# Performance work log

Hardware: AMD Instinct MI355X
Metric: run time of the kernel (lower is better)

The kernel has to match this reference:

```python
import jax, jax.numpy as jnp
import numpy as np

T, N, F_IN = 5, 10000, 16
E = 160000
C = 32          # gat_hidden_dim (per head)
H0 = 2          # heads in layer 0 (concat) -> out 64
GRU = 64
OUT_H = 32


def setup_inputs() -> dict:
    key = jax.random.key(0)
    ks = jax.random.split(key, 24)
    s = 0.1
    inp = {
        "x_seq": jax.random.normal(ks[0], (T, N, F_IN), jnp.float32),
        "edge_index": jax.random.randint(ks[1], (2, E), 0, N, jnp.int32),
        # GAT layer 0: in 16 -> 2 heads x 32, concat -> 64
        "gat0_W": s * jax.random.normal(ks[2], (F_IN, H0 * C), jnp.float32),
        "gat0_asrc": s * jax.random.normal(ks[3], (H0, C), jnp.float32),
        "gat0_adst": s * jax.random.normal(ks[4], (H0, C), jnp.float32),
        "gat0_b": s * jax.random.normal(ks[5], (H0 * C,), jnp.float32),
        "res0_W": s * jax.random.normal(ks[6], (F_IN, H0 * C), jnp.float32),   # [in,out]
        # GAT layer 1: in 64 -> 1 head x 32, no concat -> 32
        "gat1_W": s * jax.random.normal(ks[7], (H0 * C, C), jnp.float32),
        "gat1_asrc": s * jax.random.normal(ks[8], (1, C), jnp.float32),
        "gat1_adst": s * jax.random.normal(ks[9], (1, C), jnp.float32),
        "gat1_b": s * jax.random.normal(ks[10], (C,), jnp.float32),
        "res1_W": s * jax.random.normal(ks[11], (H0 * C, C), jnp.float32),
        # GRU cells (torch GRUCell layout: W_i [3H,in], W_h [3H,H])
        "gru0_Wi": s * jax.random.normal(ks[12], (3 * GRU, C), jnp.float32),
        "gru0_Wh": s * jax.random.normal(ks[13], (3 * GRU, GRU), jnp.float32),
        "gru0_bi": s * jax.random.normal(ks[14], (3 * GRU,), jnp.float32),
        "gru0_bh": s * jax.random.normal(ks[15], (3 * GRU,), jnp.float32),
        "gru1_Wi": s * jax.random.normal(ks[16], (3 * GRU, GRU), jnp.float32),
        "gru1_Wh": s * jax.random.normal(ks[17], (3 * GRU, GRU), jnp.float32),
        "gru1_bi": s * jax.random.normal(ks[18], (3 * GRU,), jnp.float32),
        "gru1_bh": s * jax.random.normal(ks[19], (3 * GRU,), jnp.float32),
        # MLP head
        "fc1_W": s * jax.random.normal(ks[20], (GRU, OUT_H), jnp.float32),
        "fc1_b": s * jax.random.normal(ks[21], (OUT_H,), jnp.float32),
        "fc2_W": s * jax.random.normal(ks[22], (OUT_H, 1), jnp.float32),
        "fc2_b": s * jax.random.normal(ks[23], (1,), jnp.float32),
    }
    return inp


def _gat(x, src, dst, n, W, a_src, a_dst, b, heads, concat):
    ch = W.shape[1] // heads
    xw = (x @ W).reshape(n, heads, ch)                      # [N,H,C]
    al_s = (xw * a_src).sum(-1)                             # [N,H]
    al_d = (xw * a_dst).sum(-1)
    e = jax.nn.leaky_relu(al_s[src] + al_d[dst], 0.2)       # [Etot,H]
    m = jax.ops.segment_max(e, dst, num_segments=n)
    ex = jnp.exp(e - m[dst])
    den = jax.ops.segment_sum(ex, dst, num_segments=n)
    alpha = ex / (den[dst] + 1e-16)                         # scatter-softmax
    out = jax.ops.segment_sum(alpha[:, :, None] * xw[src], dst, num_segments=n)
    out = out.reshape(n, heads * ch) if concat else out.mean(axis=1)
    return out + b


def _gru(x, h, Wi, Wh, bi, bh):
    gi = x @ Wi.T + bi
    gh = h @ Wh.T + bh
    i_r, i_z, i_n = jnp.split(gi, 3, axis=-1)
    h_r, h_z, h_n = jnp.split(gh, 3, axis=-1)
    r = jax.nn.sigmoid(i_r + h_r)
    z = jax.nn.sigmoid(i_z + h_z)
    nn_ = jnp.tanh(i_n + r * h_n)
    return (1.0 - z) * nn_ + z * h


def reference(x_seq, edge_index,
              gat0_W, gat0_asrc, gat0_adst, gat0_b, res0_W,
              gat1_W, gat1_asrc, gat1_adst, gat1_b, res1_W,
              gru0_Wi, gru0_Wh, gru0_bi, gru0_bh,
              gru1_Wi, gru1_Wh, gru1_bi, gru1_bh,
              fc1_W, fc1_b, fc2_W, fc2_b):
    n = x_seq.shape[1]
    loops = jnp.arange(n, dtype=edge_index.dtype)
    src = jnp.concatenate([edge_index[0], loops])           # PyG adds self-loops
    dst = jnp.concatenate([edge_index[1], loops])

    def step(carry, x_t):
        h0, h1 = carry
        x1 = jax.nn.elu(_gat(x_t, src, dst, n, gat0_W, gat0_asrc, gat0_adst, gat0_b, 2, True)) + x_t @ res0_W
        x2 = jax.nn.elu(_gat(x1, src, dst, n, gat1_W, gat1_asrc, gat1_adst, gat1_b, 1, False)) + x1 @ res1_W
        h0 = _gru(x2, h0, gru0_Wi, gru0_Wh, gru0_bi, gru0_bh)
        h1 = _gru(h0, h1, gru1_Wi, gru1_Wh, gru1_bi, gru1_bh)
        return (h0, h1), None

    h0 = jnp.zeros((n, gru0_Wh.shape[1]), x_seq.dtype)
    h1 = jnp.zeros((n, gru1_Wh.shape[1]), x_seq.dtype)
    (h0, h1), _ = jax.lax.scan(step, (h0, h1), x_seq)
    h = jax.nn.relu(h1 @ fc1_W + fc1_b)
    return h @ fc2_W + fc2_b                                # [N,1]
```

## Files before the change

### kernel.cpp

```cpp
#include <hip/hip_runtime.h>
#include <hip/hip_bf16.h>
#include <math.h>

#define T_STEPS 5
#define NNODES  10000
#define NM      (T_STEPS * NNODES)
#define F_IN    16
#define NEDGES  160000
#define ETOT    (NEDGES + NNODES)
#define GW      8
#define GNPW    5

#define RL(v, k) __int_as_float(__builtin_amdgcn_readlane(__float_as_int(v), (k)))

__global__ __launch_bounds__(256) void k_count(const int* __restrict__ ei, int* __restrict__ counts) {
    int idx = blockIdx.x * 256 + threadIdx.x;
    if (idx >= ETOT) return;
    int dst = (idx < NEDGES) ? ei[NEDGES + idx] : (idx - NEDGES);
    atomicAdd(&counts[dst], 1);
}

__global__ __launch_bounds__(1024) void k_scan(const int* __restrict__ counts, int* __restrict__ offs) {
    __shared__ int ssum[1024];
    int t = threadIdx.x;
    const int chunk = (NNODES + 1023) / 1024;
    int start = t * chunk, end = min(start + chunk, NNODES);
    int s = 0;
    for (int i = start; i < end; i++) s += counts[i];
    ssum[t] = s;
    __syncthreads();
    for (int off = 1; off < 1024; off <<= 1) {
        int v = (t >= off) ? ssum[t - off] : 0;
        __syncthreads();
        ssum[t] += v;
        __syncthreads();
    }
    int excl = (t == 0) ? 0 : ssum[t - 1];
    for (int i = start; i < end; i++) { offs[i] = excl; excl += counts[i]; }
    if (t == 1023) offs[NNODES] = ssum[1023];
}

__global__ __launch_bounds__(256) void k_fill(const int* __restrict__ ei, const int* __restrict__ offs,
                                              int* __restrict__ cursor, int* __restrict__ csr) {
    int idx = blockIdx.x * 256 + threadIdx.x;
    if (idx >= ETOT) return;
    int src, dst;
    if (idx < NEDGES) { src = ei[idx]; dst = ei[NEDGES + idx]; }
    else              { src = dst = idx - NEDGES; }
    int p = atomicAdd(&cursor[dst], 1);
    csr[offs[dst] + p] = src;
}

__global__ __launch_bounds__(256) void k_transpose(const float* __restrict__ Wi0, const float* __restrict__ Wh0,
                                                   const float* __restrict__ Wi1, const float* __restrict__ Wh1,
                                                   float* __restrict__ WiT0, float* __restrict__ WhT0,
                                                   float* __restrict__ WiT1, float* __restrict__ WhT1,
                                                   float4* __restrict__ wp0, float4* __restrict__ hp0,
                                                   float4* __restrict__ ip1, float4* __restrict__ hp1) {
    int idx = blockIdx.x * 256 + threadIdx.x;
    if (idx < 6144)  { int k = idx / 192, r = idx % 192; WiT0[idx] = Wi0[r * 32 + k]; return; }
    idx -= 6144;
    if (idx < 12288) { int k = idx / 192, r = idx % 192; WhT0[idx] = Wh0[r * 64 + k]; return; }
    idx -= 12288;
    if (idx < 12288) { int k = idx / 192, r = idx % 192; WiT1[idx] = Wi1[r * 64 + k]; return; }
    idx -= 12288;
    if (idx < 12288) { int k = idx / 192, r = idx % 192; WhT1[idx] = Wh1[r * 64 + k]; return; }
    idx -= 12288;
    if (idx < 1536) { int k4 = idx / 192, c = idx % 192; const float* s = Wi0 + c * 32 + 4 * k4;
                      wp0[idx] = make_float4(s[0], s[1], s[2], s[3]); return; }
    idx -= 1536;
    if (idx < 3072) { int k4 = idx / 192, c = idx % 192; const float* s = Wh0 + c * 64 + 4 * k4;
                      hp0[idx] = make_float4(s[0], s[1], s[2], s[3]); return; }
    idx -= 3072;
    if (idx < 3072) { int k4 = idx / 192, c = idx % 192; const float* s = Wi1 + c * 64 + 4 * k4;
                      ip1[idx] = make_float4(s[0], s[1], s[2], s[3]); return; }
    idx -= 3072;
    if (idx < 3072) { int k4 = idx / 192, c = idx % 192; const float* s = Wh1 + c * 64 + 4 * k4;
                      hp1[idx] = make_float4(s[0], s[1], s[2], s[3]); }
}

__global__ __launch_bounds__(256) void k_mm0_all(const float* __restrict__ x,
                                                 const float* __restrict__ W,
                                                 const float* __restrict__ Wres,
                                                 const float* __restrict__ asrc,
                                                 const float* __restrict__ adst,
                                                 float* __restrict__ xw, float* __restrict__ xres,
                                                 float* __restrict__ als, float* __restrict__ ald) {
    int wave = threadIdx.x >> 6, lane = threadIdx.x & 63;
    int m = blockIdx.x * 4 + wave;
    if (m >= NM) return;
    const float* xr = x + (size_t)m * F_IN;
    float xreg[F_IN];
#pragma unroll
    for (int k = 0; k < F_IN; k++) xreg[k] = xr[k];
    float acc = 0.f, accr = 0.f;
#pragma unroll
    for (int k = 0; k < F_IN; k++) {
        acc  += xreg[k] * W[k * 64 + lane];
        accr += xreg[k] * Wres[k * 64 + lane];
    }
    xw[(size_t)m * 64 + lane]   = acc;
    xres[(size_t)m * 64 + lane] = accr;
    float ps = acc * asrc[lane], pd = acc * adst[lane];
    for (int off = 16; off; off >>= 1) {
        ps += __shfl_down(ps, off, 32);
        pd += __shfl_down(pd, off, 32);
    }
    if ((lane & 31) == 0) {
        int h = lane >> 5;
        als[m * 2 + h] = ps;
        ald[m * 2 + h] = pd;
    }
}

__global__ __launch_bounds__(256) void k_gat0_all(const float* __restrict__ xw,
                                                  const float* __restrict__ xres,
                                                  const float* __restrict__ als,
                                                  const float* __restrict__ ald,
                                                  const int* __restrict__ offs, const int* __restrict__ csr,
                                                  const float* __restrict__ b,
                                                  const float* __restrict__ W1,
                                                  const float* __restrict__ Wres1,
                                                  const float* __restrict__ as1,
                                                  const float* __restrict__ ad1v,
                                                  float* __restrict__ xw1, float* __restrict__ xres1,
                                                  float* __restrict__ als1, float* __restrict__ ald1) {
    int wave = threadIdx.x >> 6, lane = threadIdx.x & 63;
    int m = blockIdx.x * 4 + wave;
    if (m >= NM) return;
    int t = m / NNODES;
    int node = m - t * NNODES;
    int base = t * NNODES;
    int beg = offs[node], end = offs[node + 1];
    int deg = end - beg;
    float ad0 = ald[m * 2 + 0], ad1 = ald[m * 2 + 1];
    float acc;
    if (deg <= 64) {
        int s = 0; float e0 = -INFINITY, e1 = -INFINITY;
        if (lane < deg) {
            s = base + csr[beg + lane];
            e0 = als[s * 2 + 0] + ad0; e0 = e0 > 0.f ? e0 : 0.2f * e0;
            e1 = als[s * 2 + 1] + ad1; e1 = e1 > 0.f ? e1 : 0.2f * e1;
        }
        float m0 = e0, m1 = e1;
        for (int o = 32; o; o >>= 1) {
            m0 = fmaxf(m0, __shfl_xor(m0, o));
            m1 = fmaxf(m1, __shfl_xor(m1, o));
        }
        float ex0 = (lane < deg) ? __expf(e0 - m0) : 0.f;
        float ex1 = (lane < deg) ? __expf(e1 - m1) : 0.f;
        float d0 = ex0, d1 = ex1;
        for (int o = 32; o; o >>= 1) {
            d0 += __shfl_xor(d0, o);
            d1 += __shfl_xor(d1, o);
        }
        ex0 *= 1.f / (d0 + 1e-16f);
        ex1 *= 1.f / (d1 + 1e-16f);
        float a0 = 0.f, a1 = 0.f, a2 = 0.f, a3 = 0.f;
        int i = 0;
        for (; i + 4 <= deg; i += 4) {
            int   s0 = __shfl(s, i),     s1 = __shfl(s, i + 1), s2 = __shfl(s, i + 2), s3 = __shfl(s, i + 3);
            float u0 = __shfl(ex0, i),   v0 = __shfl(ex1, i);
            float u1 = __shfl(ex0, i+1), v1 = __shfl(ex1, i+1);
            float u2 = __shfl(ex0, i+2), v2 = __shfl(ex1, i+2);
            float u3 = __shfl(ex0, i+3), v3 = __shfl(ex1, i+3);
            a0 += (lane < 32 ? u0 : v0) * xw[(size_t)s0 * 64 + lane];
            a1 += (lane < 32 ? u1 : v1) * xw[(size_t)s1 * 64 + lane];
            a2 += (lane < 32 ? u2 : v2) * xw[(size_t)s2 * 64 + lane];
            a3 += (lane < 32 ? u3 : v3) * xw[(size_t)s3 * 64 + lane];
        }
        for (; i < deg; i++) {
            int s0 = __shfl(s, i);
            float u = __shfl(ex0, i), v = __shfl(ex1, i);
            a0 += (lane < 32 ? u : v) * xw[(size_t)s0 * 64 + lane];
        }
        acc = (a0 + a1) + (a2 + a3);
    } else {
        float m0 = -INFINITY, m1 = -INFINITY;
        for (int i = beg + lane; i < end; i += 64) {
            int s = base + csr[i];
            float e0 = als[s * 2 + 0] + ad0; e0 = e0 > 0.f ? e0 : 0.2f * e0;
            float e1 = als[s * 2 + 1] + ad1; e1 = e1 > 0.f ? e1 : 0.2f * e1;
            m0 = fmaxf(m0, e0); m1 = fmaxf(m1, e1);
        }
        for (int o = 32; o; o >>= 1) {
            m0 = fmaxf(m0, __shfl_xor(m0, o));
            m1 = fmaxf(m1, __shfl_xor(m1, o));
        }
        float d0 = 0.f, d1 = 0.f;
        for (int i = beg + lane; i < end; i += 64) {
            int s = base + csr[i];
            float e0 = als[s * 2 + 0] + ad0; e0 = e0 > 0.f ? e0 : 0.2f * e0;
            float e1 = als[s * 2 + 1] + ad1; e1 = e1 > 0.f ? e1 : 0.2f * e1;
            d0 += __expf(e0 - m0); d1 += __expf(e1 - m1);
        }
        for (int o = 32; o; o >>= 1) { d0 += __shfl_xor(d0, o); d1 += __shfl_xor(d1, o); }
        float inv0 = 1.f / (d0 + 1e-16f), inv1 = 1.f / (d1 + 1e-16f);
        acc = 0.f;
        for (int i = beg; i < end; i++) {
            int s = base + csr[i];
            float e, wgt;
            if (lane < 32) { e = als[s * 2 + 0] + ad0; e = e > 0.f ? e : 0.2f * e; wgt = __expf(e - m0) * inv0; }
            else           { e = als[s * 2 + 1] + ad1; e = e > 0.f ? e : 0.2f * e; wgt = __expf(e - m1) * inv1; }
            acc += wgt * xw[(size_t)s * 64 + lane];
        }
    }
    float x1v = acc + b[lane];
    x1v = x1v > 0.f ? x1v : expm1f(x1v);
    x1v += xres[(size_t)m * 64 + lane];
    int j = lane & 31;
    const float* Wp = (lane < 32) ? W1 : Wres1;
    float pacc = 0.f;
#pragma unroll
    for (int k = 0; k < 64; k++) {
        float xv = RL(x1v, k);
        pacc += xv * Wp[k * 32 + j];
    }
    if (lane < 32) xw1[(size_t)m * 32 + j]   = pacc;
    else           xres1[(size_t)m * 32 + j] = pacc;
    float ps = (lane < 32) ? pacc * as1[j]  : 0.f;
    float pd = (lane < 32) ? pacc * ad1v[j] : 0.f;
    for (int o = 16; o; o >>= 1) {
        ps += __shfl_down(ps, o, 32);
        pd += __shfl_down(pd, o, 32);
    }
    if (lane == 0) { als1[m] = ps; ald1[m] = pd; }
}

__global__ __launch_bounds__(256) void k_gat1_all(const float* __restrict__ xw1,
                                                  const float* __restrict__ xres1,
                                                  const float* __restrict__ als1,
                                                  const float* __restrict__ ald1,
                                                  const int* __restrict__ offs, const int* __restrict__ csr,
                                                  const float* __restrict__ b,
                                                  float* __restrict__ x2) {
    int wave = threadIdx.x >> 6, lane = threadIdx.x & 63;
    int m = blockIdx.x * 4 + wave;
    if (m >= NM) return;
    int t = m / NNODES;
    int node = m - t * NNODES;
    int base = t * NNODES;
    int beg = offs[node], end = offs[node + 1];
    int deg = end - beg;
    float adv = ald1[m];
    int ch = lane & 31, half = lane >> 5;
    float aggr;
    if (deg <= 64) {
        int s = 0; float e = -INFINITY;
        if (lane < deg) {
            s = base + csr[beg + lane];
            e = als1[s] + adv; e = e > 0.f ? e : 0.2f * e;
        }
        float mx = e;
        for (int o = 32; o; o >>= 1) mx = fmaxf(mx, __shfl_xor(mx, o));
        float ex = (lane < deg) ? __expf(e - mx) : 0.f;
        float d = ex;
        for (int o = 32; o; o >>= 1) d += __shfl_xor(d, o);
        ex *= 1.f / (d + 1e-16f);
        float acc = 0.f;
        for (int i = 0; i < deg; i += 2) {
            int i2 = (i + 1 < deg) ? i + 1 : i;
            int   sa = __shfl(s, i),  sb = __shfl(s, i2);
            float wa = __shfl(ex, i), wb = __shfl(ex, i2);
            if (i + 1 >= deg) wb = 0.f;
            int   sm = half ? sb : sa;
            float wm = half ? wb : wa;
            acc += wm * xw1[(size_t)sm * 32 + ch];
        }
        acc += __shfl_xor(acc, 32);
        aggr = acc;
    } else {
        float mx = -INFINITY;
        for (int i = beg + lane; i < end; i += 64) {
            float e = als1[base + csr[i]] + adv; e = e > 0.f ? e : 0.2f * e;
            mx = fmaxf(mx, e);
        }
        for (int o = 32; o; o >>= 1) mx = fmaxf(mx, __shfl_xor(mx, o));
        float d = 0.f;
        for (int i = beg + lane; i < end; i += 64) {
            float e = als1[base + csr[i]] + adv; e = e > 0.f ? e : 0.2f * e;
            d += __expf(e - mx);
        }
        for (int o = 32; o; o >>= 1) d += __shfl_xor(d, o);
        float inv = 1.f / (d + 1e-16f);
        float acc = 0.f;
        for (int i = beg; i < end; i++) {
            int s = base + csr[i];
            float e = als1[s] + adv; e = e > 0.f ? e : 0.2f * e;
            float wgt = __expf(e - mx) * inv;
            acc += wgt * xw1[(size_t)s * 32 + ch];
        }
        aggr = acc;
    }
    if (lane < 32) {
        float v = aggr + b[ch];
        v = v > 0.f ? v : expm1f(v);
        x2[(size_t)m * 32 + ch] = v + xres1[(size_t)m * 32 + ch];
    }
}

__global__ __launch_bounds__(512) void k_gruhead_p(const float* __restrict__ x2,
                                                   const float4* __restrict__ wp0,
                                                   const float4* __restrict__ hp0,
                                                   const float4* __restrict__ ip1,
                                                   const float4* __restrict__ hp1,
                                                   const float* __restrict__ bi0, const float* __restrict__ bh0,
                                                   const float* __restrict__ bi1, const float* __restrict__ bh1,
                                                   const float* __restrict__ fc1W, const float* __restrict__ fc1b,
                                                   const float* __restrict__ fc2W, const float* __restrict__ fc2b,
                                                   float* __restrict__ out) {
    extern __shared__ float4 lds4[];
    float4* Lh0 = lds4;
    float4* Li1 = lds4 + 3072;
    float4* Lh1 = lds4 + 6144;
    int tid = threadIdx.x, wave = tid >> 6, lane = tid & 63;
    int node0 = (blockIdx.x * GW + wave) * GNPW;

    for (int i = tid; i < 3072; i += 512) { Lh0[i] = hp0[i]; Li1[i] = ip1[i]; Lh1[i] = hp1[i]; }
    __syncthreads();

    float bir0 = bi0[lane] + bh0[lane];
    float biz0 = bi0[64 + lane] + bh0[64 + lane];
    float bin0 = bi0[128 + lane], bhn0 = bh0[128 + lane];
    float bir1 = bi1[lane] + bh1[lane];
    float biz1 = bi1[64 + lane] + bh1[64 + lane];
    float bin1 = bi1[128 + lane], bhn1 = bh1[128 + lane];

    float h0[GNPW] = {0.f, 0.f, 0.f, 0.f, 0.f};
    float h1[GNPW] = {0.f, 0.f, 0.f, 0.f, 0.f};

    for (int t = 0; t < T_STEPS; t++) {
        size_t rb = ((size_t)t * NNODES + node0) * 32;
        float xa = x2[rb + lane];
        float xb = x2[rb + 64 + lane];
        float xc = x2[rb + 128 + (lane & 31)];

        float gr[GNPW], gz[GNPW], gin[GNPW], ghn[GNPW];
#pragma unroll
        for (int n = 0; n < GNPW; n++) { gr[n] = bir0; gz[n] = biz0; gin[n] = bin0; ghn[n] = bhn0; }
#pragma unroll
        for (int k4 = 0; k4 < 8; k4++) {
            float4 wr = wp0[(k4 * 3 + 0) * 64 + lane];
            float4 wz = wp0[(k4 * 3 + 1) * 64 + lane];
            float4 wn = wp0[(k4 * 3 + 2) * 64 + lane];
            int kb = 4 * k4;
#pragma unroll
            for (int n = 0; n < GNPW; n++) {
                float x0, x1, x2v, x3;
                if      (n == 0) { x0 = RL(xa, kb); x1 = RL(xa, kb+1); x2v = RL(xa, kb+2); x3 = RL(xa, kb+3); }
                else if (n == 1) { x0 = RL(xa, 32+kb); x1 = RL(xa, 33+kb); x2v = RL(xa, 34+kb); x3 = RL(xa, 35+kb); }
                else if (n == 2) { x0 = RL(xb, kb); x1 = RL(xb, kb+1); x2v = RL(xb, kb+2); x3 = RL(xb, kb+3); }
                else if (n == 3) { x0 = RL(xb, 32+kb); x1 = RL(xb, 33+kb); x2v = RL(xb, 34+kb); x3 = RL(xb, 35+kb); }
                else             { x0 = RL(xc, kb); x1 = RL(xc, kb+1); x2v = RL(xc, kb+2); x3 = RL(xc, kb+3); }
                gr[n]  += x0 * wr.x + x1 * wr.y + x2v * wr.z + x3 * wr.w;
                gz[n]  += x0 * wz.x + x1 * wz.y + x2v * wz.z + x3 * wz.w;
                gin[n] += x0 * wn.x + x1 * wn.y + x2v * wn.z + x3 * wn.w;
            }
        }
#pragma unroll 4
        for (int k4 = 0; k4 < 16; k4++) {
            float4 wr = Lh0[(k4 * 3 + 0) * 64 + lane];
            float4 wz = Lh0[(k4 * 3 + 1) * 64 + lane];
            float4 wn = Lh0[(k4 * 3 + 2) * 64 + lane];
            int kb = 4 * k4;
#pragma unroll
            for (int n = 0; n < GNPW; n++) {
                float x0 = RL(h0[n], kb), x1 = RL(h0[n], kb+1), x2v = RL(h0[n], kb+2), x3 = RL(h0[n], kb+3);
                gr[n]  += x0 * wr.x + x1 * wr.y + x2v * wr.z + x3 * wr.w;
                gz[n]  += x0 * wz.x + x1 * wz.y + x2v * wz.z + x3 * wz.w;
                ghn[n] += x0 * wn.x + x1 * wn.y + x2v * wn.z + x3 * wn.w;
            }
        }
#pragma unroll
        for (int n = 0; n < GNPW; n++) {
            float r = 1.f / (1.f + __expf(-gr[n]));
            float z = 1.f / (1.f + __expf(-gz[n]));
            float nn = tanhf(gin[n] + r * ghn[n]);
            h0[n] = (1.f - z) * nn + z * h0[n];
        }

#pragma unroll
        for (int n = 0; n < GNPW; n++) { gr[n] = bir1; gz[n] = biz1; gin[n] = bin1; }
#pragma unroll 4
        for (int k4 = 0; k4 < 16; k4++) {
            float4 wr = Li1[(k4 * 3 + 0) * 64 + lane];
            float4 wz = Li1[(k4 * 3 + 1) * 64 + lane];
            float4 wn = Li1[(k4 * 3 + 2) * 64 + lane];
            int kb = 4 * k4;
#pragma unroll
            for (int n = 0; n < GNPW; n++) {
                float x0 = RL(h0[n], kb), x1 = RL(h0[n], kb+1), x2v = RL(h0[n], kb+2), x3 = RL(h0[n], kb+3);
                gr[n]  += x0 * wr.x + x1 * wr.y + x2v * wr.z + x3 * wr.w;
                gz[n]  += x0 * wz.x + x1 * wz.y + x2v * wz.z + x3 * wz.w;
                gin[n] += x0 * wn.x + x1 * wn.y + x2v * wn.z + x3 * wn.w;
            }
        }
#pragma unroll
        for (int n = 0; n < GNPW; n++) ghn[n] = bhn1;
#pragma unroll 4
        for (int k4 = 0; k4 < 16; k4++) {
            float4 wr = Lh1[(k4 * 3 + 0) * 64 + lane];
            float4 wz = Lh1[(k4 * 3 + 1) * 64 + lane];
            float4 wn = Lh1[(k4 * 3 + 2) * 64 + lane];
            int kb = 4 * k4;
#pragma unroll
            for (int n = 0; n < GNPW; n++) {
                float x0 = RL(h1[n], kb), x1 = RL(h1[n], kb+1), x2v = RL(h1[n], kb+2), x3 = RL(h1[n], kb+3);
                gr[n]  += x0 * wr.x + x1 * wr.y + x2v * wr.z + x3 * wr.w;
                gz[n]  += x0 * wz.x + x1 * wz.y + x2v * wz.z + x3 * wz.w;
                ghn[n] += x0 * wn.x + x1 * wn.y + x2v * wn.z + x3 * wn.w;
            }
        }
#pragma unroll
        for (int n = 0; n < GNPW; n++) {
            float r = 1.f / (1.f + __expf(-gr[n]));
            float z = 1.f / (1.f + __expf(-gz[n]));
            float nn = tanhf(gin[n] + r * ghn[n]);
            h1[n] = (1.f - z) * nn + z * h1[n];
        }
    }

    int j = lane & 31, half = lane >> 5;
#pragma unroll
    for (int p = 0; p < 3; p++) {
        int ne = 2 * p;
        int no = (2 * p + 1 < GNPW) ? 2 * p + 1 : 2 * p;
        float a = fc1b[j];
#pragma unroll
        for (int k = 0; k < 64; k++) {
            float he = RL(h1[ne], k);
            float ho = RL(h1[no], k);
            a += (half ? ho : he) * fc1W[k * 32 + j];
        }
        a = fmaxf(a, 0.f);
        float v = a * fc2W[j];
        for (int o = 16; o; o >>= 1) v += __shfl_down(v, o, 32);
        if ((lane & 31) == 0 && 2 * p + half < GNPW) out[node0 + 2 * p + half] = v + fc2b[0];
    }
}

__global__ __launch_bounds__(512) void k_gruhead(const float* __restrict__ x2,
                                                 const float* __restrict__ WiT0,
                                                 const float* __restrict__ WhT0,
                                                 const float* __restrict__ WiT1,
                                                 const float* __restrict__ WhT1,
                                                 const float* __restrict__ bi0, const float* __restrict__ bh0,
                                                 const float* __restrict__ bi1, const float* __restrict__ bh1,
                                                 const float* __restrict__ fc1W, const float* __restrict__ fc1b,
                                                 const float* __restrict__ fc2W, const float* __restrict__ fc2b,
                                                 float* __restrict__ out) {
    __shared__ float lw[64 * 192];
    int tid = threadIdx.x;
    int wave = tid >> 6, lane = tid & 63;
    int node0 = (blockIdx.x * GW + wave) * GNPW;

    float bir0 = bi0[lane] + bh0[lane];
    float biz0 = bi0[64 + lane] + bh0[64 + lane];
    float bin0 = bi0[128 + lane], bhn0 = bh0[128 + lane];
    float bir1 = bi1[lane] + bh1[lane];
    float biz1 = bi1[64 + lane] + bh1[64 + lane];
    float bin1 = bi1[128 + lane], bhn1 = bh1[128 + lane];

    float h0[GNPW] = {0.f, 0.f, 0.f, 0.f, 0.f};
    float h1[GNPW] = {0.f, 0.f, 0.f, 0.f, 0.f};

    auto stage = [&](const float* __restrict__ src) {
        __syncthreads();
        const float4* s4 = (const float4*)src;
        float4* d4 = (float4*)lw;
#pragma unroll
        for (int i = 0; i < 6; i++) d4[tid + i * 512] = s4[tid + i * 512];
        __syncthreads();
    };

    for (int t = 0; t < T_STEPS; t++) {
        size_t rb = ((size_t)t * NNODES + node0) * 32;
        float xa = x2[rb + lane];
        float xb = x2[rb + 64 + lane];
        float xc = x2[rb + 128 + (lane & 31)];

        float gr[GNPW], gz[GNPW], gin[GNPW], ghn[GNPW];
#pragma unroll
        for (int n = 0; n < GNPW; n++) { gr[n] = bir0; gz[n] = biz0; gin[n] = bin0; ghn[n] = bhn0; }
#pragma unroll 4
        for (int k = 0; k < 32; k++) {
            float wr = WiT0[k * 192 + lane];
            float wz = WiT0[k * 192 + 64 + lane];
            float wn = WiT0[k * 192 + 128 + lane];
            float xv[GNPW];
            xv[0] = RL(xa, k); xv[1] = RL(xa, 32 + k);
            xv[2] = RL(xb, k); xv[3] = RL(xb, 32 + k);
            xv[4] = RL(xc, k);
#pragma unroll
            for (int n = 0; n < GNPW; n++) {
                gr[n] += xv[n] * wr; gz[n] += xv[n] * wz; gin[n] += xv[n] * wn;
            }
        }
        stage(WhT0);
#pragma unroll 4
        for (int k = 0; k < 64; k++) {
            float wr = lw[k * 192 + lane];
            float wz = lw[k * 192 + 64 + lane];
            float wn = lw[k * 192 + 128 + lane];
#pragma unroll
            for (int n = 0; n < GNPW; n++) {
                float hv = RL(h0[n], k);
                gr[n] += hv * wr; gz[n] += hv * wz; ghn[n] += hv * wn;
            }
        }
#pragma unroll
        for (int n = 0; n < GNPW; n++) {
            float r = 1.f / (1.f + __expf(-gr[n]));
            float z = 1.f / (1.f + __expf(-gz[n]));
            float nn = tanhf(gin[n] + r * ghn[n]);
            h0[n] = (1.f - z) * nn + z * h0[n];
        }
#pragma unroll
        for (int n = 0; n < GNPW; n++) { gr[n] = bir1; gz[n] = biz1; gin[n] = bin1; }
        stage(WiT1);
#pragma unroll 4
        for (int k = 0; k < 64; k++) {
            float wir = lw[k * 192 + lane];
            float wiz = lw[k * 192 + 64 + lane];
            float win = lw[k * 192 + 128 + lane];
#pragma unroll
            for (int n = 0; n < GNPW; n++) {
                float xv = RL(h0[n], k);
                gr[n] += xv * wir; gz[n] += xv * wiz; gin[n] += xv * win;
            }
        }
#pragma unroll
        for (int n = 0; n < GNPW; n++) ghn[n] = bhn1;
        stage(WhT1);
#pragma unroll 4
        for (int k = 0; k < 64; k++) {
            float whr = lw[k * 192 + lane];
            float whz = lw[k * 192 + 64 + lane];
            float whn = lw[k * 192 + 128 + lane];
#pragma unroll
            for (int n = 0; n < GNPW; n++) {
                float hv = RL(h1[n], k);
                gr[n] += hv * whr; gz[n] += hv * whz; ghn[n] += hv * whn;
            }
        }
#pragma unroll
        for (int n = 0; n < GNPW; n++) {
            float r = 1.f / (1.f + __expf(-gr[n]));
            float z = 1.f / (1.f + __expf(-gz[n]));
            float nn = tanhf(gin[n] + r * ghn[n]);
            h1[n] = (1.f - z) * nn + z * h1[n];
        }
    }

    int j = lane & 31, half = lane >> 5;
#pragma unroll
    for (int p = 0; p < 3; p++) {
        int ne = 2 * p;
        int no = (2 * p + 1 < GNPW) ? 2 * p + 1 : 2 * p;
        float a = fc1b[j];
#pragma unroll
        for (int k = 0; k < 64; k++) {
            float he = RL(h1[ne], k);
            float ho = RL(h1[no], k);
            a += (half ? ho : he) * fc1W[k * 32 + j];
        }
        a = fmaxf(a, 0.f);
        float v = a * fc2W[j];
        for (int o = 16; o; o >>= 1) v += __shfl_down(v, o, 32);
        if ((lane & 31) == 0 && 2 * p + half < GNPW) out[node0 + 2 * p + half] = v + fc2b[0];
    }
}

extern "C" void kernel_launch(void* const* d_in, const int* in_sizes, int n_in,
                              void* d_out, int out_size, void* d_ws, size_t ws_size,
                              hipStream_t stream) {
    const float* x_seq   = (const float*)d_in[0];
    const int*   ei      = (const int*)d_in[1];
    const float* gat0_W  = (const float*)d_in[2];
    const float* gat0_as = (const float*)d_in[3];
    const float* gat0_ad = (const float*)d_in[4];
    const float* gat0_b  = (const float*)d_in[5];
    const float* res0_W  = (const float*)d_in[6];
    const float* gat1_W  = (const float*)d_in[7];
    const float* gat1_as = (const float*)d_in[8];
    const float* gat1_ad = (const float*)d_in[9];
    const float* gat1_b  = (const float*)d_in[10];
    const float* res1_W  = (const float*)d_in[11];
    const float* gru0_Wi = (const float*)d_in[12];
    const float* gru0_Wh = (const float*)d_in[13];
    const float* gru0_bi = (const float*)d_in[14];
    const float* gru0_bh = (const float*)d_in[15];
    const float* gru1_Wi = (const float*)d_in[16];
    const float* gru1_Wh = (const float*)d_in[17];
    const float* gru1_bi = (const float*)d_in[18];
    const float* gru1_bh = (const float*)d_in[19];
    const float* fc1_W   = (const float*)d_in[20];
    const float* fc1_b   = (const float*)d_in[21];
    const float* fc2_W   = (const float*)d_in[22];
    const float* fc2_b   = (const float*)d_in[23];
    float* out = (float*)d_out;

    char* w = (char*)d_ws;
    size_t off = 0;
    auto take = [&](size_t bytes) { size_t r = off; off += (bytes + 255) & ~(size_t)255; return r; };
    const size_t N = NNODES, M = NM;
    int*    counts = (int*)(w + take(N * 4));
    int*    cursor = (int*)(w + take(N * 4));
    int*    offs   = (int*)(w + take((N + 1) * 4));
    int*    csr    = (int*)(w + take((size_t)ETOT * 4));
    float*  xw0    = (float*)(w + take(M * 64 * 4));
    float*  xres0  = (float*)(w + take(M * 64 * 4));
    float*  als0   = (float*)(w + take(M * 2 * 4));
    float*  ald0   = (float*)(w + take(M * 2 * 4));
    float*  xw1    = (float*)(w + take(M * 32 * 4));
    float*  xres1  = (float*)(w + take(M * 32 * 4));
    float*  als1   = (float*)(w + take(M * 4));
    float*  ald1   = (float*)(w + take(M * 4));
    float*  x2     = (float*)(w + take(M * 32 * 4));
    float*  wiT0   = (float*)(w + take(32 * 192 * 4));
    float*  whT0   = (float*)(w + take(64 * 192 * 4));
    float*  wiT1   = (float*)(w + take(64 * 192 * 4));
    float*  whT1   = (float*)(w + take(64 * 192 * 4));
    float4* wp0    = (float4*)(w + take(1536 * 16));
    float4* hp0    = (float4*)(w + take(3072 * 16));
    float4* ip1    = (float4*)(w + take(3072 * 16));
    float4* hp1    = (float4*)(w + take(3072 * 16));

    hipMemsetAsync(counts, 0, N * 4, stream);
    hipMemsetAsync(cursor, 0, N * 4, stream);
    const int egrid = (ETOT + 255) / 256;
    k_count<<<egrid, 256, 0, stream>>>(ei, counts);
    k_scan<<<1, 1024, 0, stream>>>(counts, offs);
    k_fill<<<egrid, 256, 0, stream>>>(ei, offs, cursor, csr);
    const int ttot = 6144 + 3 * 12288 + 1536 + 3 * 3072;
    k_transpose<<<(ttot + 255) / 256, 256, 0, stream>>>(gru0_Wi, gru0_Wh, gru1_Wi, gru1_Wh,
                                                        wiT0, whT0, wiT1, whT1,
                                                        wp0, hp0, ip1, hp1);

    const int mgrid = (NM + 3) / 4;
    k_mm0_all<<<mgrid, 256, 0, stream>>>(x_seq, gat0_W, res0_W, gat0_as, gat0_ad, xw0, xres0, als0, ald0);
    k_gat0_all<<<mgrid, 256, 0, stream>>>(xw0, xres0, als0, ald0, offs, csr, gat0_b,
                                          gat1_W, res1_W, gat1_as, gat1_ad,
                                          xw1, xres1, als1, ald1);
    k_gat1_all<<<mgrid, 256, 0, stream>>>(xw1, xres1, als1, ald1, offs, csr, gat1_b, x2);

    const int ggrid = NNODES / (GW * GNPW);
    hipError_t ae = hipFuncSetAttribute(reinterpret_cast<const void*>(k_gruhead_p),
                                        hipFuncAttributeMaxDynamicSharedMemorySize, 147456);
    if (ae == hipSuccess) {
        k_gruhead_p<<<ggrid, 512, 147456, stream>>>(x2, wp0, hp0, ip1, hp1,
                                                    gru0_bi, gru0_bh, gru1_bi, gru1_bh,
                                                    fc1_W, fc1_b, fc2_W, fc2_b, out);
    } else {
        k_gruhead<<<ggrid, 512, 0, stream>>>(x2, wiT0, whT0, wiT1, whT1,
                                             gru0_bi, gru0_bh, gru1_bi, gru1_bh,
                                             fc1_W, fc1_b, fc2_W, fc2_b, out);
    }
}
```

Before: 380.7 us.

## Fuse GRU0 input projection into GAT1 kernel and simplify GRU weight layout

The GRU layer-0 input projection (x2·Wi0 + bi0) moves into the GAT1 epilogue, where each wave computes all 192 gate pre-activations per node and writes gi0 instead of x2. The serial GRU kernel then reads precomputed gates and does only the recurrent matmuls, taking work off the low-parallelism recurrent kernel. In exchange, intermediate traffic grows sixfold (192 floats per node-step instead of 32). The float4-packed LDS weight layout is also replaced by plain transposed scalar layouts, which means more LDS load instructions in the inner loops.

```diff
diff --git a/kernel.cpp b/kernel.cpp
--- a/kernel.cpp
+++ b/kernel.cpp
@@ -54,9 +54,7 @@
 __global__ __launch_bounds__(256) void k_transpose(const float* __restrict__ Wi0, const float* __restrict__ Wh0,
                                                    const float* __restrict__ Wi1, const float* __restrict__ Wh1,
                                                    float* __restrict__ WiT0, float* __restrict__ WhT0,
-                                                   float* __restrict__ WiT1, float* __restrict__ WhT1,
-                                                   float4* __restrict__ wp0, float4* __restrict__ hp0,
-                                                   float4* __restrict__ ip1, float4* __restrict__ hp1) {
+                                                   float* __restrict__ WiT1, float* __restrict__ WhT1) {
     int idx = blockIdx.x * 256 + threadIdx.x;
     if (idx < 6144)  { int k = idx / 192, r = idx % 192; WiT0[idx] = Wi0[r * 32 + k]; return; }
     idx -= 6144;
@@ -64,19 +62,7 @@
     idx -= 12288;
     if (idx < 12288) { int k = idx / 192, r = idx % 192; WiT1[idx] = Wi1[r * 64 + k]; return; }
     idx -= 12288;
-    if (idx < 12288) { int k = idx / 192, r = idx % 192; WhT1[idx] = Wh1[r * 64 + k]; return; }
-    idx -= 12288;
-    if (idx < 1536) { int k4 = idx / 192, c = idx % 192; const float* s = Wi0 + c * 32 + 4 * k4;
-                      wp0[idx] = make_float4(s[0], s[1], s[2], s[3]); return; }
-    idx -= 1536;
-    if (idx < 3072) { int k4 = idx / 192, c = idx % 192; const float* s = Wh0 + c * 64 + 4 * k4;
-                      hp0[idx] = make_float4(s[0], s[1], s[2], s[3]); return; }
-    idx -= 3072;
-    if (idx < 3072) { int k4 = idx / 192, c = idx % 192; const float* s = Wi1 + c * 64 + 4 * k4;
-                      ip1[idx] = make_float4(s[0], s[1], s[2], s[3]); return; }
-    idx -= 3072;
-    if (idx < 3072) { int k4 = idx / 192, c = idx % 192; const float* s = Wh1 + c * 64 + 4 * k4;
-                      hp1[idx] = make_float4(s[0], s[1], s[2], s[3]); }
+    if (idx < 12288) { int k = idx / 192, r = idx % 192; WhT1[idx] = Wh1[r * 64 + k]; }
 }
 
 __global__ __launch_bounds__(256) void k_mm0_all(const float* __restrict__ x,
@@ -233,7 +219,9 @@
                                                   const float* __restrict__ ald1,
                                                   const int* __restrict__ offs, const int* __restrict__ csr,
                                                   const float* __restrict__ b,
-                                                  float* __restrict__ x2) {
+                                                  const float* __restrict__ WiT0,
+                                                  const float* __restrict__ bi0,
+                                                  float* __restrict__ gi0) {
     int wave = threadIdx.x >> 6, lane = threadIdx.x & 63;
     int m = blockIdx.x * 4 + wave;
     if (m >= NM) return;
@@ -292,36 +280,51 @@
         }
         aggr = acc;
     }
-    if (lane < 32) {
-        float v = aggr + b[ch];
-        v = v > 0.f ? v : expm1f(v);
-        x2[(size_t)m * 32 + ch] = v + xres1[(size_t)m * 32 + ch];
-    }
-}
-
-__global__ __launch_bounds__(512) void k_gruhead_p(const float* __restrict__ x2,
-                                                   const float4* __restrict__ wp0,
-                                                   const float4* __restrict__ hp0,
-                                                   const float4* __restrict__ ip1,
-                                                   const float4* __restrict__ hp1,
-                                                   const float* __restrict__ bi0, const float* __restrict__ bh0,
+    float v = aggr + b[ch];
+    v = v > 0.f ? v : expm1f(v);
+    float x2v = v + xres1[(size_t)m * 32 + ch];
+#pragma unroll
+    for (int p = 0; p < 3; p++) {
+        float accp = bi0[p * 64 + lane];
+#pragma unroll 8
+        for (int k = 0; k < 32; k++) {
+            accp += RL(x2v, k) * WiT0[k * 192 + p * 64 + lane];
+        }
+        gi0[(size_t)m * 192 + p * 64 + lane] = accp;
+    }
+}
+
+__global__ __launch_bounds__(512) void k_gruhead_p(const float* __restrict__ gi0,
+                                                   const float* __restrict__ WhT0,
+                                                   const float* __restrict__ WiT1,
+                                                   const float* __restrict__ WhT1,
+                                                   const float* __restrict__ bh0,
                                                    const float* __restrict__ bi1, const float* __restrict__ bh1,
                                                    const float* __restrict__ fc1W, const float* __restrict__ fc1b,
                                                    const float* __restrict__ fc2W, const float* __restrict__ fc2b,
                                                    float* __restrict__ out) {
-    extern __shared__ float4 lds4[];
-    float4* Lh0 = lds4;
-    float4* Li1 = lds4 + 3072;
-    float4* Lh1 = lds4 + 6144;
+    extern __shared__ float lds[];
+    float* Lh0 = lds;
+    float* Li1 = lds + 12288;
+    float* Lh1 = lds + 24576;
     int tid = threadIdx.x, wave = tid >> 6, lane = tid & 63;
     int node0 = (blockIdx.x * GW + wave) * GNPW;
 
-    for (int i = tid; i < 3072; i += 512) { Lh0[i] = hp0[i]; Li1[i] = ip1[i]; Lh1[i] = hp1[i]; }
+    {
+        const float4* a = (const float4*)WhT0;
+        const float4* bsrc = (const float4*)WiT1;
+        const float4* c = (const float4*)WhT1;
+        float4* A = (float4*)Lh0; float4* B = (float4*)Li1; float4* C = (float4*)Lh1;
+#pragma unroll
+        for (int i = 0; i < 6; i++) {
+            A[tid + i * 512] = a[tid + i * 512];
+            B[tid + i * 512] = bsrc[tid + i * 512];
+            C[tid + i * 512] = c[tid + i * 512];
+        }
+    }
     __syncthreads();
 
-    float bir0 = bi0[lane] + bh0[lane];
-    float biz0 = bi0[64 + lane] + bh0[64 + lane];
-    float bin0 = bi0[128 + lane], bhn0 = bh0[128 + lane];
+    float bhr0 = bh0[lane], bhz0 = bh0[64 + lane], bhn0 = bh0[128 + lane];
     float bir1 = bi1[lane] + bh1[lane];
     float biz1 = bi1[64 + lane] + bh1[64 + lane];
     float bin1 = bi1[128 + lane], bhn1 = bh1[128 + lane];
@@ -330,45 +333,24 @@
     float h1[GNPW] = {0.f, 0.f, 0.f, 0.f, 0.f};
 
     for (int t = 0; t < T_STEPS; t++) {
-        size_t rb = ((size_t)t * NNODES + node0) * 32;
-        float xa = x2[rb + lane];
-        float xb = x2[rb + 64 + lane];
-        float xc = x2[rb + 128 + (lane & 31)];
-
         float gr[GNPW], gz[GNPW], gin[GNPW], ghn[GNPW];
-#pragma unroll
-        for (int n = 0; n < GNPW; n++) { gr[n] = bir0; gz[n] = biz0; gin[n] = bin0; ghn[n] = bhn0; }
-#pragma unroll
-        for (int k4 = 0; k4 < 8; k4++) {
-            float4 wr = wp0[(k4 * 3 + 0) * 64 + lane];
-            float4 wz = wp0[(k4 * 3 + 1) * 64 + lane];
-            float4 wn = wp0[(k4 * 3 + 2) * 64 + lane];
-            int kb = 4 * k4;
+        size_t gb = ((size_t)t * NNODES + node0) * 192;
+#pragma unroll
+        for (int n = 0; n < GNPW; n++) {
+            gr[n]  = gi0[gb + n * 192 + lane] + bhr0;
+            gz[n]  = gi0[gb + n * 192 + 64 + lane] + bhz0;
+            gin[n] = gi0[gb + n * 192 + 128 + lane];
+            ghn[n] = bhn0;
+        }
+#pragma unroll 4
+        for (int k = 0; k < 64; k++) {
+            float wr = Lh0[k * 192 + lane];
+            float wz = Lh0[k * 192 + 64 + lane];
+            float wn = Lh0[k * 192 + 128 + lane];
 #pragma unroll
             for (int n = 0; n < GNPW; n++) {
-                float x0, x1, x2v, x3;
-                if      (n == 0) { x0 = RL(xa, kb); x1 = RL(xa, kb+1); x2v = RL(xa, kb+2); x3 = RL(xa, kb+3); }
-                else if (n == 1) { x0 = RL(xa, 32+kb); x1 = RL(xa, 33+kb); x2v = RL(xa, 34+kb); x3 = RL(xa, 35+kb); }
-                else if (n == 2) { x0 = RL(xb, kb); x1 = RL(xb, kb+1); x2v = RL(xb, kb+2); x3 = RL(xb, kb+3); }
-                else if (n == 3) { x0 = RL(xb, 32+kb); x1 = RL(xb, 33+kb); x2v = RL(xb, 34+kb); x3 = RL(xb, 35+kb); }
-                else             { x0 = RL(xc, kb); x1 = RL(xc, kb+1); x2v = RL(xc, kb+2); x3 = RL(xc, kb+3); }
-                gr[n]  += x0 * wr.x + x1 * wr.y + x2v * wr.z + x3 * wr.w;
-                gz[n]  += x0 * wz.x + x1 * wz.y + x2v * wz.z + x3 * wz.w;
-                gin[n] += x0 * wn.x + x1 * wn.y + x2v * wn.z + x3 * wn.w;
-            }
-        }
-#pragma unroll 4
-        for (int k4 = 0; k4 < 16; k4++) {
-            float4 wr = Lh0[(k4 * 3 + 0) * 64 + lane];
-            float4 wz = Lh0[(k4 * 3 + 1) * 64 + lane];
-            float4 wn = Lh0[(k4 * 3 + 2) * 64 + lane];
-            int kb = 4 * k4;
-#pragma unroll
-            for (int n = 0; n < GNPW; n++) {
-                float x0 = RL(h0[n], kb), x1 = RL(h0[n], kb+1), x2v = RL(h0[n], kb+2), x3 = RL(h0[n], kb+3);
-                gr[n]  += x0 * wr.x + x1 * wr.y + x2v * wr.z + x3 * wr.w;
-                gz[n]  += x0 * wz.x + x1 * wz.y + x2v * wz.z + x3 * wz.w;
-                ghn[n] += x0 * wn.x + x1 * wn.y + x2v * wn.z + x3 * wn.w;
+                float hv = RL(h0[n], k);
+                gr[n] += hv * wr; gz[n] += hv * wz; ghn[n] += hv * wn;
             }
         }
 #pragma unroll
@@ -382,33 +364,27 @@
 #pragma unroll
         for (int n = 0; n < GNPW; n++) { gr[n] = bir1; gz[n] = biz1; gin[n] = bin1; }
 #pragma unroll 4
-        for (int k4 = 0; k4 < 16; k4++) {
-            float4 wr = Li1[(k4 * 3 + 0) * 64 + lane];
-            float4 wz = Li1[(k4 * 3 + 1) * 64 + lane];
-            float4 wn = Li1[(k4 * 3 + 2) * 64 + lane];
-            int kb = 4 * k4;
+        for (int k = 0; k < 64; k++) {
+            float wir = Li1[k * 192 + lane];
+            float wiz = Li1[k * 192 + 64 + lane];
+            float win = Li1[k * 192 + 128 + lane];
 #pragma unroll
             for (int n = 0; n < GNPW; n++) {
-                float x0 = RL(h0[n], kb), x1 = RL(h0[n], kb+1), x2v = RL(h0[n], kb+2), x3 = RL(h0[n], kb+3);
-                gr[n]  += x0 * wr.x + x1 * wr.y + x2v * wr.z + x3 * wr.w;
-                gz[n]  += x0 * wz.x + x1 * wz.y + x2v * wz.z + x3 * wz.w;
-                gin[n] += x0 * wn.x + x1 * wn.y + x2v * wn.z + x3 * wn.w;
+                float xv = RL(h0[n], k);
+                gr[n] += xv * wir; gz[n] += xv * wiz; gin[n] += xv * win;
             }
         }
 #pragma unroll
         for (int n = 0; n < GNPW; n++) ghn[n] = bhn1;
 #pragma unroll 4
-        for (int k4 = 0; k4 < 16; k4++) {
-            float4 wr = Lh1[(k4 * 3 + 0) * 64 + lane];
-            float4 wz = Lh1[(k4 * 3 + 1) * 64 + lane];
-            float4 wn = Lh1[(k4 * 3 + 2) * 64 + lane];
-            int kb = 4 * k4;
+        for (int k = 0; k < 64; k++) {
+            float whr = Lh1[k * 192 + lane];
+            float whz = Lh1[k * 192 + 64 + lane];
+            float whn = Lh1[k * 192 + 128 + lane];
 #pragma unroll
             for (int n = 0; n < GNPW; n++) {
-                float x0 = RL(h1[n], kb), x1 = RL(h1[n], kb+1), x2v = RL(h1[n], kb+2), x3 = RL(h1[n], kb+3);
-                gr[n]  += x0 * wr.x + x1 * wr.y + x2v * wr.z + x3 * wr.w;
-                gz[n]  += x0 * wz.x + x1 * wz.y + x2v * wz.z + x3 * wz.w;
-                ghn[n] += x0 * wn.x + x1 * wn.y + x2v * wn.z + x3 * wn.w;
+                float hv = RL(h1[n], k);
+                gr[n] += hv * whr; gz[n] += hv * whz; ghn[n] += hv * whn;
             }
         }
 #pragma unroll
@@ -439,12 +415,11 @@
     }
 }
 
-__global__ __launch_bounds__(512) void k_gruhead(const float* __restrict__ x2,
-                                                 const float* __restrict__ WiT0,
+__global__ __launch_bounds__(512) void k_gruhead(const float* __restrict__ gi0,
                                                  const float* __restrict__ WhT0,
                                                  const float* __restrict__ WiT1,
                                                  const float* __restrict__ WhT1,
-                                                 const float* __restrict__ bi0, const float* __restrict__ bh0,
+                                                 const float* __restrict__ bh0,
                                                  const float* __restrict__ bi1, const float* __restrict__ bh1,
                                                  const float* __restrict__ fc1W, const float* __restrict__ fc1b,
                                                  const float* __restrict__ fc2W, const float* __restrict__ fc2b,
@@ -454,9 +429,7 @@
     int wave = tid >> 6, lane = tid & 63;
     int node0 = (blockIdx.x * GW + wave) * GNPW;
 
-    float bir0 = bi0[lane] + bh0[lane];
-    float biz0 = bi0[64 + lane] + bh0[64 + lane];
-    float bin0 = bi0[128 + lane], bhn0 = bh0[128 + lane];
+    float bhr0 = bh0[lane], bhz0 = bh0[64 + lane], bhn0 = bh0[128 + lane];
     float bir1 = bi1[lane] + bh1[lane];
     float biz1 = bi1[64 + lane] + bh1[64 + lane];
     float bin1 = bi1[128 + lane], bhn1 = bh1[128 + lane];
@@ -474,27 +447,14 @@
     };
 
     for (int t = 0; t < T_STEPS; t++) {
-        size_t rb = ((size_t)t * NNODES + node0) * 32;
-        float xa = x2[rb + lane];
-        float xb = x2[rb + 64 + lane];
-        float xc = x2[rb + 128 + (lane & 31)];
-
         float gr[GNPW], gz[GNPW], gin[GNPW], ghn[GNPW];
-#pragma unroll
-        for (int n = 0; n < GNPW; n++) { gr[n] = bir0; gz[n] = biz0; gin[n] = bin0; ghn[n] = bhn0; }
-#pragma unroll 4
-        for (int k = 0; k < 32; k++) {
-            float wr = WiT0[k * 192 + lane];
-            float wz = WiT0[k * 192 + 64 + lane];
-            float wn = WiT0[k * 192 + 128 + lane];
-            float xv[GNPW];
-            xv[0] = RL(xa, k); xv[1] = RL(xa, 32 + k);
-            xv[2] = RL(xb, k); xv[3] = RL(xb, 32 + k);
-            xv[4] = RL(xc, k);
-#pragma unroll
-            for (int n = 0; n < GNPW; n++) {
-                gr[n] += xv[n] * wr; gz[n] += xv[n] * wz; gin[n] += xv[n] * wn;
-            }
+        size_t gb = ((size_t)t * NNODES + node0) * 192;
+#pragma unroll
+        for (int n = 0; n < GNPW; n++) {
+            gr[n]  = gi0[gb + n * 192 + lane] + bhr0;
+            gz[n]  = gi0[gb + n * 192 + 64 + lane] + bhz0;
+            gin[n] = gi0[gb + n * 192 + 128 + lane];
+            ghn[n] = bhn0;
         }
         stage(WhT0);
 #pragma unroll 4
@@ -604,27 +564,23 @@
     size_t off = 0;
     auto take = [&](size_t bytes) { size_t r = off; off += (bytes + 255) & ~(size_t)255; return r; };
     const size_t N = NNODES, M = NM;
-    int*    counts = (int*)(w + take(N * 4));
-    int*    cursor = (int*)(w + take(N * 4));
-    int*    offs   = (int*)(w + take((N + 1) * 4));
-    int*    csr    = (int*)(w + take((size_t)ETOT * 4));
-    float*  xw0    = (float*)(w + take(M * 64 * 4));
-    float*  xres0  = (float*)(w + take(M * 64 * 4));
-    float*  als0   = (float*)(w + take(M * 2 * 4));
-    float*  ald0   = (float*)(w + take(M * 2 * 4));
-    float*  xw1    = (float*)(w + take(M * 32 * 4));
-    float*  xres1  = (float*)(w + take(M * 32 * 4));
-    float*  als1   = (float*)(w + take(M * 4));
-    float*  ald1   = (float*)(w + take(M * 4));
-    float*  x2     = (float*)(w + take(M * 32 * 4));
-    float*  wiT0   = (float*)(w + take(32 * 192 * 4));
-    float*  whT0   = (float*)(w + take(64 * 192 * 4));
-    float*  wiT1   = (float*)(w + take(64 * 192 * 4));
-    float*  whT1   = (float*)(w + take(64 * 192 * 4));
-    float4* wp0    = (float4*)(w + take(1536 * 16));
-    float4* hp0    = (float4*)(w + take(3072 * 16));
-    float4* ip1    = (float4*)(w + take(3072 * 16));
-    float4* hp1    = (float4*)(w + take(3072 * 16));
+    int*   counts = (int*)(w + take(N * 4));
+    int*   cursor = (int*)(w + take(N * 4));
+    int*   offs   = (int*)(w + take((N + 1) * 4));
+    int*   csr    = (int*)(w + take((size_t)ETOT * 4));
+    float* xw0    = (float*)(w + take(M * 64 * 4));
+    float* xres0  = (float*)(w + take(M * 64 * 4));
+    float* als0   = (float*)(w + take(M * 2 * 4));
+    float* ald0   = (float*)(w + take(M * 2 * 4));
+    float* xw1    = (float*)(w + take(M * 32 * 4));
+    float* xres1  = (float*)(w + take(M * 32 * 4));
+    float* als1   = (float*)(w + take(M * 4));
+    float* ald1   = (float*)(w + take(M * 4));
+    float* gi0    = (float*)(w + take(M * 192 * 4));
+    float* wiT0   = (float*)(w + take(32 * 192 * 4));
+    float* whT0   = (float*)(w + take(64 * 192 * 4));
+    float* wiT1   = (float*)(w + take(64 * 192 * 4));
+    float* whT1   = (float*)(w + take(64 * 192 * 4));
 
     hipMemsetAsync(counts, 0, N * 4, stream);
     hipMemsetAsync(cursor, 0, N * 4, stream);
@@ -632,28 +588,28 @@
     k_count<<<egrid, 256, 0, stream>>>(ei, counts);
     k_scan<<<1, 1024, 0, stream>>>(counts, offs);
     k_fill<<<egrid, 256, 0, stream>>>(ei, offs, cursor, csr);
-    const int ttot = 6144 + 3 * 12288 + 1536 + 3 * 3072;
+    const int ttot = 6144 + 3 * 12288;
     k_transpose<<<(ttot + 255) / 256, 256, 0, stream>>>(gru0_Wi, gru0_Wh, gru1_Wi, gru1_Wh,
-                                                        wiT0, whT0, wiT1, whT1,
-                                                        wp0, hp0, ip1, hp1);
+                                                        wiT0, whT0, wiT1, whT1);
 
     const int mgrid = (NM + 3) / 4;
     k_mm0_all<<<mgrid, 256, 0, stream>>>(x_seq, gat0_W, res0_W, gat0_as, gat0_ad, xw0, xres0, als0, ald0);
     k_gat0_all<<<mgrid, 256, 0, stream>>>(xw0, xres0, als0, ald0, offs, csr, gat0_b,
                                           gat1_W, res1_W, gat1_as, gat1_ad,
                                           xw1, xres1, als1, ald1);
-    k_gat1_all<<<mgrid, 256, 0, stream>>>(xw1, xres1, als1, ald1, offs, csr, gat1_b, x2);
+    k_gat1_all<<<mgrid, 256, 0, stream>>>(xw1, xres1, als1, ald1, offs, csr, gat1_b,
+                                          wiT0, gru0_bi, gi0);
 
     const int ggrid = NNODES / (GW * GNPW);
     hipError_t ae = hipFuncSetAttribute(reinterpret_cast<const void*>(k_gruhead_p),
                                         hipFuncAttributeMaxDynamicSharedMemorySize, 147456);
     if (ae == hipSuccess) {
-        k_gruhead_p<<<ggrid, 512, 147456, stream>>>(x2, wp0, hp0, ip1, hp1,
-                                                    gru0_bi, gru0_bh, gru1_bi, gru1_bh,
+        k_gruhead_p<<<ggrid, 512, 147456, stream>>>(gi0, whT0, wiT1, whT1,
+                                                    gru0_bh, gru1_bi, gru1_bh,
                                                     fc1_W, fc1_b, fc2_W, fc2_b, out);
     } else {
-        k_gruhead<<<ggrid, 512, 0, stream>>>(x2, wiT0, whT0, wiT1, whT1,
-                                             gru0_bi, gru0_bh, gru1_bi, gru1_bh,
+        k_gruhead<<<ggrid, 512, 0, stream>>>(gi0, whT0, wiT1, whT1,
+                                             gru0_bh, gru1_bi, gru1_bh,
                                              fc1_W, fc1_b, fc2_W, fc2_b, out);
     }
 }
```

After: 382.1 us. About the same (+0.4%).
